# Kernel tuning notes

Measured on AMD Instinct MI355X. Metric: run time of the kernel, lower is better.

Reference implementation:

```python
import jax, jax.numpy as jnp
import numpy as np

B, S, H, OUT = 512, 128, 512, 1
IN = 1
P = 0.1  # drop_rate


def setup_inputs() -> dict:
    key = jax.random.key(0)
    ks = jax.random.split(key, 14)
    x = jax.random.normal(ks[0], (B, S), dtype=jnp.float32)
    # Bayesian LSTM variational params (blitz-style: W = mu + log1p(exp(rho)) * eps)
    W_ih_mu = jax.random.normal(ks[1], (IN, 4 * H), dtype=jnp.float32) * 0.1
    W_ih_rho = jnp.full((IN, 4 * H), -5.0, dtype=jnp.float32)
    eps_ih = jax.random.normal(ks[2], (IN, 4 * H), dtype=jnp.float32)
    W_hh_mu = jax.random.normal(ks[3], (H, 4 * H), dtype=jnp.float32) * 0.1
    W_hh_rho = jnp.full((H, 4 * H), -5.0, dtype=jnp.float32)
    eps_hh = jax.random.normal(ks[4], (H, 4 * H), dtype=jnp.float32)
    b_mu = jax.random.normal(ks[5], (4 * H,), dtype=jnp.float32) * 0.1
    b_rho = jnp.full((4 * H,), -5.0, dtype=jnp.float32)
    eps_b = jax.random.normal(ks[6], (4 * H,), dtype=jnp.float32)
    # linear head
    W_lin = jax.random.normal(ks[7], (H, OUT), dtype=jnp.float32) * 0.05
    b_lin = jnp.zeros((OUT,), dtype=jnp.float32)
    # dropout masks (training=True always); pre-scaled inverted dropout
    keep = 1.0 - P
    mask_in = jax.random.bernoulli(ks[8], keep, (B, S, 1)).astype(jnp.float32) / keep
    # second dropout is applied to hidden_seq then sliced at t=-1, so only the
    # last-step mask matters
    mask_out = jax.random.bernoulli(ks[9], keep, (B, H)).astype(jnp.float32) / keep
    return {
        "x": x,
        "W_ih_mu": W_ih_mu, "W_ih_rho": W_ih_rho, "eps_ih": eps_ih,
        "W_hh_mu": W_hh_mu, "W_hh_rho": W_hh_rho, "eps_hh": eps_hh,
        "b_mu": b_mu, "b_rho": b_rho, "eps_b": eps_b,
        "W_lin": W_lin, "b_lin": b_lin,
        "mask_in": mask_in, "mask_out": mask_out,
    }


def reference(x, W_ih_mu, W_ih_rho, eps_ih, W_hh_mu, W_hh_rho, eps_hh,
              b_mu, b_rho, eps_b, W_lin, b_lin, mask_in, mask_out):
    # reparameterized weight samples
    W_ih = W_ih_mu + jnp.log1p(jnp.exp(W_ih_rho)) * eps_ih   # (IN, 4H)
    W_hh = W_hh_mu + jnp.log1p(jnp.exp(W_hh_rho)) * eps_hh   # (H, 4H)
    b = b_mu + jnp.log1p(jnp.exp(b_rho)) * eps_b             # (4H,)

    # reshape (B,S) -> (B,S,1) + input dropout
    xr = x[:, :, None] * mask_in                              # (B,S,1)
    # input projection for all timesteps at once
    x_proj = jnp.einsum('bsi,ih->bsh', xr, W_ih) + b          # (B,S,4H)
    xs = jnp.swapaxes(x_proj, 0, 1)                           # (S,B,4H)

    h0 = jnp.zeros((B, H), dtype=x.dtype)
    c0 = jnp.zeros((B, H), dtype=x.dtype)

    def step(carry, gx):
        h, c = carry
        gates = gx + h @ W_hh                                 # (B,4H)
        i_g, f_g, g_g, o_g = jnp.split(gates, 4, axis=-1)
        i_t = jax.nn.sigmoid(i_g)
        f_t = jax.nn.sigmoid(f_g)
        g_t = jnp.tanh(g_g)
        o_t = jax.nn.sigmoid(o_g)
        c_new = f_t * c + i_t * g_t
        h_new = o_t * jnp.tanh(c_new)
        return (h_new, c_new), h_new

    (h_last, _), _ = jax.lax.scan(step, (h0, c0), xs)
    # output dropout (only last step matters after slicing), then linear head
    out = (h_last * mask_out) @ W_lin + b_lin                 # (B,OUT)
    return out
```

## Files before the change

### kernel.cpp

```cpp
#include <hip/hip_runtime.h>
#include <hip/hip_bf16.h>


typedef __attribute__((ext_vector_type(8))) _Float16 half8;
typedef __attribute__((ext_vector_type(4))) float f32x4;
typedef unsigned long long u64;
typedef unsigned int u32;

#define HID   512
#define BATCH 512
#define SEQ   128

__device__ __forceinline__ float bf2f(__hip_bfloat16 v) { return __bfloat162float(v); }
__device__ __forceinline__ float softplus_f(float x) { return log1pf(__expf(x)); }
__device__ __forceinline__ float sigm(float x) { return 1.f / (1.f + __expf(-x)); }
__device__ __forceinline__ float tanh_fast(float x) {
  x = fminf(fmaxf(x, -15.f), 15.f);
  float e = __expf(2.f * x);
  return (e - 1.f) / (e + 1.f);
}
__device__ __forceinline__ float ldin(const void* p, size_t i, int md) {
  return md ? ((const float*)p)[i] : bf2f(((const __hip_bfloat16*)p)[i]);
}
__device__ __forceinline__ int probe_md(const void* b_rho) {
  return (((const u32*)b_rho)[0] == 0xC0A00000u) ? 1 : 0;
}
__device__ __forceinline__ unsigned short f16bits(_Float16 h) {
  union { _Float16 f; unsigned short u; } c; c.f = h; return c.u;
}
__device__ __forceinline__ u64 ald64(const u64* p) {
  return __hip_atomic_load((u64*)p, __ATOMIC_RELAXED, __HIP_MEMORY_SCOPE_AGENT);
}
__device__ __forceinline__ u32 ald32(const u32* p) {
  return __hip_atomic_load((u32*)p, __ATOMIC_RELAXED, __HIP_MEMORY_SCOPE_AGENT);
}
__device__ __forceinline__ void ast32(u32* p, u32 v) {
  (void)__hip_atomic_exchange(p, v, __ATOMIC_RELAXED, __HIP_MEMORY_SCOPE_AGENT);
}
__device__ __forceinline__ void ast64(u64* p, u64 v) {
  (void)__hip_atomic_exchange(p, v, __ATOMIC_RELAXED, __HIP_MEMORY_SCOPE_AGENT);
}

__device__ __forceinline__ void pollR13(const u32* p, u32 tgt) {
  long gd = 0;
  for (;;) {
    const u32 v = ald32(p);
    if (__ballot(v >= tgt) == ~0ULL) break;
    if (++gd > 1000000L) break;
  }
}

__global__ __launch_bounds__(256) void setup_all(
    const void* __restrict__ x,
    const void* __restrict__ Wih_mu, const void* __restrict__ Wih_rho,
    const void* __restrict__ eps_ih,
    const void* __restrict__ Whh_mu, const void* __restrict__ Whh_rho,
    const void* __restrict__ eps_hh,
    const void* __restrict__ b_mu, const void* __restrict__ b_rho,
    const void* __restrict__ eps_b,
    const void* __restrict__ mask_in,
    unsigned short* __restrict__ Wtf,
    float* __restrict__ Wih4, float* __restrict__ bias4, float* __restrict__ xm,
    u32* __restrict__ hA32, u32* __restrict__ flags) {
  const int md = probe_md(b_rho);
  const int bid = blockIdx.x;
  if (bid < 512) {
    const int idx = bid * 256 + threadIdx.x;
    const int ncol = idx & 2047;
    const int kq = idx >> 11;
    const int kk = kq >> 2, q = kq & 3;
    const int g = ncol >> 9, j = ncol & 511;
    const int js = j >> 4, rr = j & 15;
    const int lane = rr + 16 * q;
    union { half8 h; unsigned short s[8]; } out;
#pragma unroll
    for (int s = 0; s < 8; ++s) {
      const size_t src = (size_t)(kk * 32 + q * 8 + s) * 2048 + ncol;
      const float w = ldin(Whh_mu, src, md) +
                      softplus_f(ldin(Whh_rho, src, md)) * ldin(eps_hh, src, md);
      out.s[s] = f16bits((_Float16)w);
    }
    *(half8*)(Wtf + (((size_t)((g * 32 + js) * 16 + kk) * 64 + lane) * 8)) = out.h;
  } else {
    const int idx = (bid - 512) * 256 + threadIdx.x;
    if (idx < 2048) {
      Wih4[idx] = ldin(Wih_mu, idx, md) +
                  softplus_f(ldin(Wih_rho, idx, md)) * ldin(eps_ih, idx, md);
    } else if (idx < 4096) {
      const int n = idx - 2048;
      bias4[n] = ldin(b_mu, n, md) + softplus_f(ldin(b_rho, n, md)) * ldin(eps_b, n, md);
    } else if (idx < 69632) {
      const int i = idx - 4096;
      const int s = i >> 9, b = i & 511;
      const size_t src = (size_t)b * SEQ + s;
      xm[(size_t)s * BATCH + b] = ldin(x, src, md) * ldin(mask_in, src, md);
    } else if (idx < 200704) {
      hA32[idx - 69632] = 0u;
    } else if (idx < 204800) {
      flags[idx - 200704] = 0u;
    }
  }
}

__global__ __launch_bounds__(512, 2) void lstm_persist(
    u64* __restrict__ hA, u64* __restrict__ hB,
    float* __restrict__ hf, const unsigned short* __restrict__ Wtf,
    const float* __restrict__ Wih4, const float* __restrict__ bias4,
    const float* __restrict__ xm, u32* __restrict__ flags,
    const void* __restrict__ mask_out, const void* __restrict__ W_lin,
    const void* __restrict__ b_lin, const void* __restrict__ b_rho,
    void* __restrict__ out) {
  __shared__ half8 WS[2048];
  __shared__ f32x4 exch[8][4][64];
  __shared__ u32 T[4][16][17];
  const int tid  = threadIdx.x;
  const int lane = tid & 63;
  const int wv   = tid >> 6;
  const int w    = wv & 3;
  const int hv   = wv >> 2;
  const int r = lane & 15, q = lane >> 4;
  const int bid = blockIdx.x;
  const int mg = bid >> 5, js = bid & 31;
  const int j0 = js * 16, m0 = mg * 64 + w * 16, mt = mg * 4 + w;
  const int md = probe_md(b_rho);

  for (int fi = tid; fi < 2048; fi += 512) {
    const int wsg = fi >> 10;
    const int kk = (fi >> 6) & 15;
    const int ln = fi & 63;
    WS[fi] = *(const half8*)(
        Wtf + (((size_t)(((wsg + 2) * 32 + js) * 16 + kk) * 64 + ln) * 8));
  }
  half8 breg[2][8];
#pragma unroll
  for (int g = 0; g < 2; ++g)
#pragma unroll
    for (int kkl = 0; kkl < 8; ++kkl)
      breg[g][kkl] = *(const half8*)(
          Wtf + (((size_t)((g * 32 + js) * 16 + hv * 8 + kkl) * 64 + lane) * 8));
  __syncthreads();

  const int jj = j0 + r;
  const float wih_i = Wih4[jj],             bi  = bias4[jj];
  const float wih_f = Wih4[HID + jj],       bfv = bias4[HID + jj];
  const float wih_g = Wih4[2 * HID + jj],   bg  = bias4[2 * HID + jj];
  const float wih_o = Wih4[3 * HID + jj],   bo  = bias4[3 * HID + jj];

  float cc0 = 0.f, cc1 = 0.f;
  u32* myflag = flags + (size_t)(mg * 32 + js) * 16;
  u32* pollp  = flags + (size_t)(mg * 32 + (lane & 31)) * 16;

  const int mtc = wv >> 1, half = wv & 1;
  const int sl = lane & 31;
  const int sri = sl & 15;
  const int sc0 = ((sl >> 4) << 3) + half * 4;
  const size_t oidx = (size_t)((mg * 4 + mtc) * 16 + (js >> 1)) * 128 +
                      (size_t)half * 64 + (size_t)(js & 1) * 32 + sl;

  for (int t = 0; t < SEQ; ++t) {
    const u64* ih = (t & 1) ? hB : hA;
    u64*       oh = (t & 1) ? hA : hB;

    const size_t rb = (size_t)(mt * 16 + hv * 8) * 128 + lane;
    u64 uh[16];
#pragma unroll
    for (int kkl = 0; kkl < 8; ++kkl) {
      uh[kkl * 2]     = ald64(ih + rb + (size_t)kkl * 128);
      uh[kkl * 2 + 1] = ald64(ih + rb + (size_t)kkl * 128 + 64);
    }

    const float xb0 = xm[t * BATCH + m0 + q * 4 + hv * 2 + 0];
    const float xb1 = xm[t * BATCH + m0 + q * 4 + hv * 2 + 1];

    f32x4 a0 = {0.f, 0.f, 0.f, 0.f};
    f32x4 a1 = a0, a2 = a0, a3 = a0;
#pragma unroll
    for (int kkl = 0; kkl < 8; ++kkl) {
      const int kk = hv * 8 + kkl;
      const half8 b2 = WS[(0 * 16 + kk) * 64 + lane];
      const half8 b3 = WS[(1 * 16 + kk) * 64 + lane];
      union { half8 h; u64 d[2]; } ah;
      ah.d[0] = uh[kkl * 2]; ah.d[1] = uh[kkl * 2 + 1];
      a0 = __builtin_amdgcn_mfma_f32_16x16x32_f16(ah.h, breg[0][kkl], a0, 0, 0, 0);
      a1 = __builtin_amdgcn_mfma_f32_16x16x32_f16(ah.h, breg[1][kkl], a1, 0, 0, 0);
      a2 = __builtin_amdgcn_mfma_f32_16x16x32_f16(ah.h, b2, a2, 0, 0, 0);
      a3 = __builtin_amdgcn_mfma_f32_16x16x32_f16(ah.h, b3, a3, 0, 0, 0);
    }

    exch[wv][0][lane] = a0; exch[wv][1][lane] = a1;
    exch[wv][2][lane] = a2; exch[wv][3][lane] = a3;
    __syncthreads();
    const int pw = wv ^ 4;
    a0 += exch[pw][0][lane]; a1 += exch[pw][1][lane];
    a2 += exch[pw][2][lane]; a3 += exch[pw][3][lane];

#pragma unroll
    for (int i2 = 0; i2 < 2; ++i2) {
      const int i = hv * 2 + i2;
      const int m = m0 + q * 4 + i;
      const float xb = i2 ? xb1 : xb0;
      const float pi = a0[i] + xb * wih_i + bi;
      const float pf = a1[i] + xb * wih_f + bfv;
      const float pg = a2[i] + xb * wih_g + bg;
      const float po = a3[i] + xb * wih_o + bo;
      const float cprev = i2 ? cc1 : cc0;
      const float cn = sigm(pf) * cprev + sigm(pi) * tanh_fast(pg);
      const float hn = sigm(po) * tanh_fast(cn);
      if (i2) cc1 = cn; else cc0 = cn;
      T[w][q * 4 + i][r] = (u32)f16bits((_Float16)hn);
      if (t == SEQ - 1)
        ast32((u32*)(hf + (size_t)m * HID + jj), __float_as_uint(hn));
    }
    __syncthreads();

    if (lane < 32) {
      const u32 x0 = T[mtc][sri][sc0];
      const u32 x1 = T[mtc][sri][sc0 + 1];
      const u32 x2 = T[mtc][sri][sc0 + 2];
      const u32 x3 = T[mtc][sri][sc0 + 3];
      const u64 hv64 = (u64)((x0 & 0xffffu) | (x1 << 16)) |
                       ((u64)((x2 & 0xffffu) | (x3 << 16)) << 32);
      ast64(oh + oidx, hv64);
    }

    if (t < SEQ - 1) {
      __syncthreads();
      if (tid == 0) ast32(myflag, (u32)(t + 1));
      if (wv == 0) pollR13(pollp, (u32)(t + 1));
      __syncthreads();
    }
  }

  __syncthreads();
  if (tid == 0) ast32(myflag, (u32)SEQ);
  if (wv == 0) pollR13(pollp, (u32)SEQ);
  __syncthreads();

  const int rA = mg * 64 + js * 2;
  const size_t iA = (size_t)rA * HID + tid;
  const size_t iB = iA + HID;
  const float hAv = __uint_as_float(ald32((const u32*)hf + iA));
  const float hBv = __uint_as_float(ald32((const u32*)hf + iB));
  float sA = hAv * ldin(mask_out, iA, md) * ldin(W_lin, tid, md);
  float sB = hBv * ldin(mask_out, iB, md) * ldin(W_lin, tid, md);
#pragma unroll
  for (int off = 32; off; off >>= 1) {
    sA += __shfl_down(sA, off, 64);
    sB += __shfl_down(sB, off, 64);
  }
  float* red = (float*)&T[0][0][0];
  if (lane == 0) { red[wv] = sA; red[8 + wv] = sB; }
  __syncthreads();
  if (tid == 0) {
    const float tA = ((red[0] + red[1]) + (red[2] + red[3])) +
                     ((red[4] + red[5]) + (red[6] + red[7]));
    const float tB = ((red[8] + red[9]) + (red[10] + red[11])) +
                     ((red[12] + red[13]) + (red[14] + red[15]));
    const float bl = ldin(b_lin, 0, md);
    if (md) {
      ((float*)out)[rA]     = tA + bl;
      ((float*)out)[rA + 1] = tB + bl;
    } else {
      ((__hip_bfloat16*)out)[rA]     = __float2bfloat16(tA + bl);
      ((__hip_bfloat16*)out)[rA + 1] = __float2bfloat16(tB + bl);
    }
  }
}

extern "C" void kernel_launch(void* const* d_in, const int* in_sizes, int n_in,
                              void* d_out, int out_size, void* d_ws, size_t ws_size,
                              hipStream_t stream) {
  const void* x        = d_in[0];
  const void* Wih_mu   = d_in[1];
  const void* Wih_rho  = d_in[2];
  const void* eps_ih   = d_in[3];
  const void* Whh_mu   = d_in[4];
  const void* Whh_rho  = d_in[5];
  const void* eps_hh   = d_in[6];
  const void* b_mu     = d_in[7];
  const void* b_rho    = d_in[8];
  const void* eps_b    = d_in[9];
  const void* W_lin    = d_in[10];
  const void* b_lin    = d_in[11];
  const void* mask_in  = d_in[12];
  const void* mask_out = d_in[13];

  char* ws = (char*)d_ws;
  unsigned short* Wtf = (unsigned short*)(ws);
  float* Wih4  = (float*)(ws + 2097152);
  float* bias4 = (float*)(ws + 2105344);
  float* xm    = (float*)(ws + 2113536);
  u64*   hA    = (u64*)(ws + 2375680);
  u64*   hB    = (u64*)(ws + 2899968);
  float* hf    = (float*)(ws + 3424256);
  u32*   flags = (u32*)(ws + 4472832);

  setup_all<<<1312, 256, 0, stream>>>(x, Wih_mu, Wih_rho, eps_ih,
                                      Whh_mu, Whh_rho, eps_hh,
                                      b_mu, b_rho, eps_b, mask_in,
                                      Wtf, Wih4, bias4, xm, (u32*)hA, flags);

  lstm_persist<<<256, 512, 0, stream>>>(hA, hB, hf, Wtf, Wih4, bias4, xm,
                                        flags, mask_out, W_lin, b_lin,
                                        b_rho, d_out);
}
```

Baseline: 575.0 us.

## Retile persistent LSTM blocks to 32 batch rows by 32 hidden columns

```diff
diff --git a/kernel.cpp b/kernel.cpp
--- a/kernel.cpp
+++ b/kernel.cpp
@@ -110,26 +110,29 @@
     const void* __restrict__ mask_out, const void* __restrict__ W_lin,
     const void* __restrict__ b_lin, const void* __restrict__ b_rho,
     void* __restrict__ out) {
-  __shared__ half8 WS[2048];
+  __shared__ half8 WS[4096];
   __shared__ f32x4 exch[8][4][64];
-  __shared__ u32 T[4][16][17];
+  __shared__ u32 T[2][2][16][17];
   const int tid  = threadIdx.x;
   const int lane = tid & 63;
   const int wv   = tid >> 6;
-  const int w    = wv & 3;
-  const int hv   = wv >> 2;
+  const int w    = wv >> 2;
+  const int c    = (wv >> 1) & 1;
+  const int hv   = wv & 1;
   const int r = lane & 15, q = lane >> 4;
   const int bid = blockIdx.x;
-  const int mg = bid >> 5, js = bid & 31;
-  const int j0 = js * 16, m0 = mg * 64 + w * 16, mt = mg * 4 + w;
+  const int mg = bid >> 4, js = bid & 15;
+  const int m0 = mg * 32 + w * 16, mt = mg * 2 + w;
+  const int jso = js * 2 + c;
   const int md = probe_md(b_rho);
 
-  for (int fi = tid; fi < 2048; fi += 512) {
-    const int wsg = fi >> 10;
-    const int kk = (fi >> 6) & 15;
-    const int ln = fi & 63;
+  for (int fi = tid; fi < 4096; fi += 512) {
+    const int cs  = fi >> 11;
+    const int wsg = (fi >> 10) & 1;
+    const int kk  = (fi >> 6) & 15;
+    const int ln  = fi & 63;
     WS[fi] = *(const half8*)(
-        Wtf + (((size_t)(((wsg + 2) * 32 + js) * 16 + kk) * 64 + ln) * 8));
+        Wtf + (((size_t)(((wsg + 2) * 32 + (js * 2 + cs)) * 16 + kk) * 64 + ln) * 8));
   }
   half8 breg[2][8];
 #pragma unroll
@@ -137,25 +140,27 @@
 #pragma unroll
     for (int kkl = 0; kkl < 8; ++kkl)
       breg[g][kkl] = *(const half8*)(
-          Wtf + (((size_t)((g * 32 + js) * 16 + hv * 8 + kkl) * 64 + lane) * 8));
+          Wtf + (((size_t)((g * 32 + jso) * 16 + hv * 8 + kkl) * 64 + lane) * 8));
   __syncthreads();
 
-  const int jj = j0 + r;
+  const int jj = jso * 16 + r;
   const float wih_i = Wih4[jj],             bi  = bias4[jj];
   const float wih_f = Wih4[HID + jj],       bfv = bias4[HID + jj];
   const float wih_g = Wih4[2 * HID + jj],   bg  = bias4[2 * HID + jj];
   const float wih_o = Wih4[3 * HID + jj],   bo  = bias4[3 * HID + jj];
 
   float cc0 = 0.f, cc1 = 0.f;
-  u32* myflag = flags + (size_t)(mg * 32 + js) * 16;
-  u32* pollp  = flags + (size_t)(mg * 32 + (lane & 31)) * 16;
-
-  const int mtc = wv >> 1, half = wv & 1;
+  u32* myflag = flags + (size_t)(mg * 16 + js) * 16;
+  u32* pollp  = flags + (size_t)(mg * 16 + (lane & 15)) * 16;
+
+  const int seg = wv & 3;
   const int sl = lane & 31;
-  const int sri = sl & 15;
-  const int sc0 = ((sl >> 4) << 3) + half * 4;
-  const size_t oidx = (size_t)((mg * 4 + mtc) * 16 + (js >> 1)) * 128 +
-                      (size_t)half * 64 + (size_t)(js & 1) * 32 + sl;
+  const int rho = sl & 15;
+  const int qq = (seg * 2 + (sl >> 4)) & 3;
+  const int dd = seg >> 1;
+  const int csrc = qq >> 1;
+  const int r0 = (qq & 1) * 8 + dd * 4;
+  const size_t oidx = ((size_t)mt * 16 + js) * 128 + seg * 32 + sl;
 
   for (int t = 0; t < SEQ; ++t) {
     const u64* ih = (t & 1) ? hB : hA;
@@ -177,8 +182,8 @@
 #pragma unroll
     for (int kkl = 0; kkl < 8; ++kkl) {
       const int kk = hv * 8 + kkl;
-      const half8 b2 = WS[(0 * 16 + kk) * 64 + lane];
-      const half8 b3 = WS[(1 * 16 + kk) * 64 + lane];
+      const half8 b2 = WS[((c * 2 + 0) * 16 + kk) * 64 + lane];
+      const half8 b3 = WS[((c * 2 + 1) * 16 + kk) * 64 + lane];
       union { half8 h; u64 d[2]; } ah;
       ah.d[0] = uh[kkl * 2]; ah.d[1] = uh[kkl * 2 + 1];
       a0 = __builtin_amdgcn_mfma_f32_16x16x32_f16(ah.h, breg[0][kkl], a0, 0, 0, 0);
@@ -190,7 +195,7 @@
     exch[wv][0][lane] = a0; exch[wv][1][lane] = a1;
     exch[wv][2][lane] = a2; exch[wv][3][lane] = a3;
     __syncthreads();
-    const int pw = wv ^ 4;
+    const int pw = wv ^ 1;
     a0 += exch[pw][0][lane]; a1 += exch[pw][1][lane];
     a2 += exch[pw][2][lane]; a3 += exch[pw][3][lane];
 
@@ -207,17 +212,17 @@
       const float cn = sigm(pf) * cprev + sigm(pi) * tanh_fast(pg);
       const float hn = sigm(po) * tanh_fast(cn);
       if (i2) cc1 = cn; else cc0 = cn;
-      T[w][q * 4 + i][r] = (u32)f16bits((_Float16)hn);
+      T[w][c][q * 4 + i][r] = (u32)f16bits((_Float16)hn);
       if (t == SEQ - 1)
         ast32((u32*)(hf + (size_t)m * HID + jj), __float_as_uint(hn));
     }
     __syncthreads();
 
     if (lane < 32) {
-      const u32 x0 = T[mtc][sri][sc0];
-      const u32 x1 = T[mtc][sri][sc0 + 1];
-      const u32 x2 = T[mtc][sri][sc0 + 2];
-      const u32 x3 = T[mtc][sri][sc0 + 3];
+      const u32 x0 = T[w][csrc][rho][r0];
+      const u32 x1 = T[w][csrc][rho][r0 + 1];
+      const u32 x2 = T[w][csrc][rho][r0 + 2];
+      const u32 x3 = T[w][csrc][rho][r0 + 3];
       const u64 hv64 = (u64)((x0 & 0xffffu) | (x1 << 16)) |
                        ((u64)((x2 & 0xffffu) | (x3 << 16)) << 32);
       ast64(oh + oidx, hv64);
@@ -236,7 +241,7 @@
   if (wv == 0) pollR13(pollp, (u32)SEQ);
   __syncthreads();
 
-  const int rA = mg * 64 + js * 2;
+  const int rA = mg * 32 + js * 2;
   const size_t iA = (size_t)rA * HID + tid;
   const size_t iB = iA + HID;
   const float hAv = __uint_as_float(ald32((const u32*)hf + iA));
@@ -248,7 +253,7 @@
     sA += __shfl_down(sA, off, 64);
     sB += __shfl_down(sB, off, 64);
   }
-  float* red = (float*)&T[0][0][0];
+  float* red = (float*)&T[0][0][0][0];
   if (lane == 0) { red[wv] = sA; red[8 + wv] = sB; }
   __syncthreads();
   if (tid == 0) {
```

Result: faster. 555.5 us, median of 2 (-3.4%).
